# Kernel tuning notes

Measured on AMD Instinct MI355X. Metric: run time of the kernel, lower is better.

Reference implementation:

```python
import jax, jax.numpy as jnp
import numpy as np

B, S, HID = 4, 2048, 2048
H, KV, D = 16, 4, 128
ROT = 32  # partial rotary dim
EPS = 1e-6
NEG = -1e9


def _rms_norm(x, w):
    # Qwen3-Next RMSNorm: fp32 norm, (1 + weight) scaling
    xf = x.astype(jnp.float32)
    out = xf * jax.lax.rsqrt(jnp.mean(xf * xf, axis=-1, keepdims=True) + EPS)
    return (out * (1.0 + w.astype(jnp.float32))).astype(x.dtype)


def _rotate_half(x):
    x1, x2 = x[..., : x.shape[-1] // 2], x[..., x.shape[-1] // 2 :]
    return jnp.concatenate((-x2, x1), axis=-1)


def setup_inputs() -> dict:
    key = jax.random.key(0)
    ks = jax.random.split(key, 8)
    hidden_states = jax.random.normal(ks[0], (B, S, HID), dtype=jnp.float32)
    # real RoPE angles for the partial rotary dims
    inv_freq = 1.0 / (10000.0 ** (np.arange(0, ROT, 2, dtype=np.float32) / ROT))
    pos = np.arange(S, dtype=np.float32)
    freqs = np.einsum('s,d->sd', pos, inv_freq)          # [S, ROT/2]
    emb = np.concatenate([freqs, freqs], axis=-1)         # [S, ROT]
    cos = jnp.broadcast_to(jnp.asarray(np.cos(emb)), (B, S, ROT))
    sin = jnp.broadcast_to(jnp.asarray(np.sin(emb)), (B, S, ROT))
    # additive causal mask [B,1,S,S]
    causal = jnp.triu(jnp.full((S, S), NEG, dtype=jnp.float32), k=1)
    attention_mask = jnp.broadcast_to(causal[None, None], (B, 1, S, S))
    std = 0.02
    wq = jax.random.normal(ks[1], (HID, H * D * 2), dtype=jnp.float32) * std
    wk = jax.random.normal(ks[2], (HID, KV * D), dtype=jnp.float32) * std
    wv = jax.random.normal(ks[3], (HID, KV * D), dtype=jnp.float32) * std
    wo = jax.random.normal(ks[4], (H * D, HID), dtype=jnp.float32) * std
    q_norm_w = jax.random.normal(ks[5], (D,), dtype=jnp.float32) * std
    k_norm_w = jax.random.normal(ks[6], (D,), dtype=jnp.float32) * std
    return {
        'hidden_states': hidden_states, 'cos': cos, 'sin': sin,
        'attention_mask': attention_mask, 'wq': wq, 'wk': wk, 'wv': wv,
        'wo': wo, 'q_norm_w': q_norm_w, 'k_norm_w': k_norm_w,
    }


def reference(hidden_states, cos, sin, attention_mask, wq, wk, wv, wo, q_norm_w, k_norm_w):
    b, s, _ = hidden_states.shape
    scaling = D ** -0.5
    # q projection -> [B,S,H,2D]; split into query and gate (chunk dim=-1)
    qg = (hidden_states @ wq).reshape(b, s, H, 2 * D)
    q, gate = qg[..., :D], qg[..., D:]
    gate = gate.reshape(b, s, H * D)
    q = _rms_norm(q, q_norm_w).transpose(0, 2, 1, 3)                    # [B,H,S,D]
    k = _rms_norm((hidden_states @ wk).reshape(b, s, KV, D), k_norm_w).transpose(0, 2, 1, 3)
    v = (hidden_states @ wv).reshape(b, s, KV, D).transpose(0, 2, 1, 3)  # [B,KV,S,D]
    # partial RoPE on first ROT dims
    c, sn = cos[:, None], sin[:, None]                                   # [B,1,S,ROT]
    q_rot, q_pass = q[..., :ROT], q[..., ROT:]
    k_rot, k_pass = k[..., :ROT], k[..., ROT:]
    q = jnp.concatenate([q_rot * c + _rotate_half(q_rot) * sn, q_pass], axis=-1)
    k = jnp.concatenate([k_rot * c + _rotate_half(k_rot) * sn, k_pass], axis=-1)
    # GQA: repeat kv heads
    groups = H // KV
    k = jnp.repeat(k, groups, axis=1)
    v = jnp.repeat(v, groups, axis=1)
    scores = jnp.einsum('bhqd,bhkd->bhqk', q, k) * scaling + attention_mask
    probs = jax.nn.softmax(scores.astype(jnp.float32), axis=-1).astype(q.dtype)
    attn = jnp.einsum('bhqk,bhkd->bhqd', probs, v)
    attn = attn.transpose(0, 2, 1, 3).reshape(b, s, H * D)
    attn = attn * jax.nn.sigmoid(gate)
    return attn @ wo
```

## Files before the change

kernel.cpp:

```cpp
#include <hip/hip_runtime.h>

#define SEQ   2048
#define NHEAD 16
#define NKV   4
#define HDIM  128
#define NB    4
#define QKVW  5120

typedef unsigned short u16;
typedef unsigned int   u32;
typedef __bf16 v8bf __attribute__((ext_vector_type(8)));
typedef float  v4f  __attribute__((ext_vector_type(4)));

__device__ __forceinline__ u16 f2bf(float f) {
  u32 u = __float_as_uint(f);
  u += 0x7fffu + ((u >> 16) & 1u);
  return (u16)(u >> 16);
}
__device__ __forceinline__ float bf2f(u16 b) {
  return __uint_as_float(((u32)b) << 16);
}

__device__ __forceinline__ void gld_lds16(const u16* g, u16* l) {
  __builtin_amdgcn_global_load_lds(
      (const __attribute__((address_space(1))) u32*)(unsigned long long)(uintptr_t)g,
      (__attribute__((address_space(3))) u32*)(u32)(uintptr_t)l,
      16, 0, 0);
}

__global__ __launch_bounds__(256) void conv_f32_bf16(const float* __restrict__ s,
                                                     u16* __restrict__ d) {
  size_t i = ((size_t)blockIdx.x * 256 + threadIdx.x) * 8;
  float4 a = *(const float4*)(s + i);
  float4 b = *(const float4*)(s + i + 4);
  uint4 o;
  o.x = (u32)f2bf(a.x) | ((u32)f2bf(a.y) << 16);
  o.y = (u32)f2bf(a.z) | ((u32)f2bf(a.w) << 16);
  o.z = (u32)f2bf(b.x) | ((u32)f2bf(b.y) << 16);
  o.w = (u32)f2bf(b.z) | ((u32)f2bf(b.w) << 16);
  *(uint4*)(d + i) = o;
}

__global__ __launch_bounds__(256) void transpose_w(const float* __restrict__ src,
                                                   u16* __restrict__ dst,
                                                   int R, int C) {
  __shared__ u16 tile[64][80];
  int t = threadIdx.x;
  int r0 = blockIdx.y * 64, c0 = blockIdx.x * 64;
  int rr = t >> 2, cc = (t & 3) * 16;
  const float* sp = src + (size_t)(r0 + rr) * C + c0 + cc;
  float4 f0 = *(const float4*)sp;
  float4 f1 = *(const float4*)(sp + 4);
  float4 f2 = *(const float4*)(sp + 8);
  float4 f3 = *(const float4*)(sp + 12);
  u16* tp = &tile[rr][cc];
  tp[0] = f2bf(f0.x);  tp[1] = f2bf(f0.y);  tp[2] = f2bf(f0.z);  tp[3] = f2bf(f0.w);
  tp[4] = f2bf(f1.x);  tp[5] = f2bf(f1.y);  tp[6] = f2bf(f1.z);  tp[7] = f2bf(f1.w);
  tp[8] = f2bf(f2.x);  tp[9] = f2bf(f2.y);  tp[10] = f2bf(f2.z); tp[11] = f2bf(f2.w);
  tp[12] = f2bf(f3.x); tp[13] = f2bf(f3.y); tp[14] = f2bf(f3.z); tp[15] = f2bf(f3.w);
  __syncthreads();
  int cr = t >> 2, rc = (t & 3) * 16;
  u32 pk[8];
#pragma unroll
  for (int i = 0; i < 8; i++) {
    u32 lo = tile[rc + 2 * i][cr];
    u32 hi = tile[rc + 2 * i + 1][cr];
    pk[i] = lo | (hi << 16);
  }
  u16* dp = dst + (size_t)(c0 + cr) * R + r0 + rc;
  uint4 o0 = {pk[0], pk[1], pk[2], pk[3]};
  uint4 o1 = {pk[4], pk[5], pk[6], pk[7]};
  *(uint4*)dp       = o0;
  *(uint4*)(dp + 8) = o1;
}

__global__ __launch_bounds__(256) void transpose_v(const u16* __restrict__ qkv,
                                                   u16* __restrict__ vt) {
  __shared__ u16 tile[64][80];
  int t = threadIdx.x;
  int s0 = blockIdx.x * 64;
  int d0 = blockIdx.y * 64;
  int bg = blockIdx.z;
  int b = bg >> 2, g = bg & 3;
  int sr = t >> 2, dc = (t & 3) * 16;
  const u16* sp = qkv + (size_t)(b * SEQ + s0 + sr) * QKVW + 4608 + g * HDIM + d0 + dc;
  *(uint4*)&tile[sr][dc]     = *(const uint4*)sp;
  *(uint4*)&tile[sr][dc + 8] = *(const uint4*)(sp + 8);
  __syncthreads();
  int dr = t >> 2, sc = (t & 3) * 16;
  u32 pk[8];
#pragma unroll
  for (int i = 0; i < 8; i++) {
    u32 lo = tile[sc + 2 * i][dr];
    u32 hi = tile[sc + 2 * i + 1][dr];
    pk[i] = lo | (hi << 16);
  }
  u16* dp = vt + ((size_t)bg * HDIM + d0 + dr) * SEQ + s0 + sc;
  uint4 o0 = {pk[0], pk[1], pk[2], pk[3]};
  uint4 o1 = {pk[4], pk[5], pk[6], pk[7]};
  *(uint4*)dp       = o0;
  *(uint4*)(dp + 8) = o1;
}

template <bool OUT_F32>
__global__ __launch_bounds__(256) void gemm_bt(const u16* __restrict__ A,
                                               const u16* __restrict__ Bt,
                                               void* __restrict__ Cp,
                                               int M, int N, int K) {
  __shared__ u16 As[2][128 * 32];
  __shared__ u16 Bs[2][128 * 32];
  int tid  = threadIdx.x;
  int lane = tid & 63, wave = tid >> 6;
  int wr = wave >> 1, wc = wave & 1;
  int col = lane & 15, quad = lane >> 4;
  int m0 = blockIdx.y * 128, n0 = blockIdx.x * 128;

  v4f acc[4][4];
#pragma unroll
  for (int mi = 0; mi < 4; mi++)
#pragma unroll
    for (int ni = 0; ni < 4; ni++) acc[mi][ni] = (v4f){0.f, 0.f, 0.f, 0.f};

  int srow = tid >> 2;
  int skc  = (tid & 3) * 8;
  const u16* ag0 = A  + (size_t)(m0 + srow) * K + skc;
  const u16* ag1 = ag0 + (size_t)64 * K;
  const u16* bg0 = Bt + (size_t)(n0 + srow) * K + skc;
  const u16* bg1 = bg0 + (size_t)64 * K;

  gld_lds16(ag0, &As[0][tid * 8]);
  gld_lds16(ag1, &As[0][2048 + tid * 8]);
  gld_lds16(bg0, &Bs[0][tid * 8]);
  gld_lds16(bg1, &Bs[0][2048 + tid * 8]);
  __syncthreads();

  int nt = K >> 5;
  for (int t = 0; t < nt; ++t) {
    int cur = t & 1, nxt = cur ^ 1;
    if (t + 1 < nt) {
      int k0 = (t + 1) << 5;
      gld_lds16(ag0 + k0, &As[nxt][tid * 8]);
      gld_lds16(ag1 + k0, &As[nxt][2048 + tid * 8]);
      gld_lds16(bg0 + k0, &Bs[nxt][tid * 8]);
      gld_lds16(bg1 + k0, &Bs[nxt][2048 + tid * 8]);
    }
    v8bf a[4], bb[4];
#pragma unroll
    for (int mi = 0; mi < 4; mi++)
      a[mi] = *(const v8bf*)&As[cur][(wr * 64 + mi * 16 + col) * 32 + quad * 8];
#pragma unroll
    for (int ni = 0; ni < 4; ni++)
      bb[ni] = *(const v8bf*)&Bs[cur][(wc * 64 + ni * 16 + col) * 32 + quad * 8];
    __builtin_amdgcn_s_setprio(1);
#pragma unroll
    for (int mi = 0; mi < 4; mi++)
#pragma unroll
      for (int ni = 0; ni < 4; ni++)
        acc[mi][ni] = __builtin_amdgcn_mfma_f32_16x16x32_bf16(a[mi], bb[ni], acc[mi][ni], 0, 0, 0);
    __builtin_amdgcn_s_setprio(0);
    __syncthreads();
  }

#pragma unroll
  for (int mi = 0; mi < 4; mi++)
#pragma unroll
    for (int ni = 0; ni < 4; ni++) {
      int r_ = m0 + wr * 64 + mi * 16 + quad * 4;
      int c_ = n0 + wc * 64 + ni * 16 + col;
#pragma unroll
      for (int r = 0; r < 4; r++) {
        if (OUT_F32) ((float*)Cp)[(size_t)(r_ + r) * N + c_] = acc[mi][ni][r];
        else         ((u16*)Cp)[(size_t)(r_ + r) * N + c_]   = f2bf(acc[mi][ni][r]);
      }
    }
}

__global__ __launch_bounds__(256) void norm_rope(u16* __restrict__ qkv,
                                                 const float* __restrict__ cosb,
                                                 const float* __restrict__ sinb,
                                                 const float* __restrict__ qw,
                                                 const float* __restrict__ kw,
                                                 u16* __restrict__ kf) {
  int wave = threadIdx.x >> 6, lane = threadIdx.x & 63;
  int tw = blockIdx.x * 4 + wave;
  int token = tw / 20, r = tw % 20;
  const u16* src;
  u16* dst;
  const float* wptr;
  if (r < 16) {
    src  = qkv + (size_t)token * QKVW + r * 256;
    dst  = (u16*)src;
    wptr = qw;
  } else {
    src  = qkv + (size_t)token * QKVW + 4096 + (r - 16) * HDIM;
    int b = token >> 11, s = token & (SEQ - 1);
    dst  = kf + ((size_t)(b * NKV + (r - 16)) * SEQ + s) * HDIM;
    wptr = kw;
  }
  int d0 = lane * 2;
  u32 x = *(const u32*)(src + d0);
  float x0 = bf2f((u16)(x & 0xffff)), x1 = bf2f((u16)(x >> 16));
  float ss = x0 * x0 + x1 * x1;
#pragma unroll
  for (int off = 1; off < 64; off <<= 1) ss += __shfl_xor(ss, off, 64);
  float sc = rsqrtf(ss * (1.f / 128.f) + 1e-6f);
  float y0 = bf2f(f2bf(x0 * sc * (1.f + wptr[d0])));
  float y1 = bf2f(f2bf(x1 * sc * (1.f + wptr[d0 + 1])));
  float p0 = __shfl_xor(y0, 8, 64);
  float p1 = __shfl_xor(y1, 8, 64);
  float z0 = y0, z1 = y1;
  if (lane < 16) {
    float c0 = cosb[(size_t)token * 32 + d0];
    float c1 = cosb[(size_t)token * 32 + d0 + 1];
    float s0 = sinb[(size_t)token * 32 + d0];
    float s1 = sinb[(size_t)token * 32 + d0 + 1];
    if (lane < 8) { z0 = y0 * c0 - p0 * s0; z1 = y1 * c1 - p1 * s1; }
    else          { z0 = y0 * c0 + p0 * s0; z1 = y1 * c1 + p1 * s1; }
  }
  u32 outp = (u32)f2bf(z0) | ((u32)f2bf(z1) << 16);
  *(u32*)(dst + d0) = outp;
}

__global__ __launch_bounds__(512) void attn_kernel(const u16* __restrict__ qkv,
                                                   const u16* __restrict__ kf,
                                                   const u16* __restrict__ vt,
                                                   u16* __restrict__ ga) {
  __shared__ u16 ks[64 * 136];
  __shared__ u16 vs[128 * 88];
  int tid = threadIdx.x, lane = tid & 63, wave = tid >> 6;
  int col = lane & 15, quad = lane >> 4;
  int qt = 15 - blockIdx.x;
  int h = blockIdx.y, b = blockIdx.z;
  int g = h >> 2;
  int qw0 = qt * 128 + wave * 16;
  int myq = qw0 + col;
  const float scl2 = 0.08838834764831845f * 1.4426950408889634f;

  v8bf qfr[4];
  const u16* qbase = qkv + (size_t)(b * SEQ + myq) * QKVW + h * 256 + quad * 8;
#pragma unroll
  for (int kc = 0; kc < 4; kc++) qfr[kc] = *(const v8bf*)(qbase + kc * 32);

  v4f o[8];
#pragma unroll
  for (int nt = 0; nt < 8; nt++) o[nt] = (v4f){0.f, 0.f, 0.f, 0.f};
  float l = 0.f;
  float m = -1e30f;

  const u16* kfb = kf + (size_t)(b * NKV + g) * SEQ * HDIM;
  const u16* vtb = vt + (size_t)(b * NKV + g) * HDIM * SEQ;

  int ksr = tid >> 4, ksd = (tid & 15) * 8;
  int vsd = tid >> 3, w8 = tid & 7;
  int voff = 32 * ((w8 >> 2) & 1) + 16 * (w8 & 1) + 4 * ((w8 >> 1) & 1);
  int vsrc = w8 * 8;

  int nk = 2 * qt + 2;
  for (int it = 0; it < nk; it++) {
    int k0 = it * 64;
    __syncthreads();
#pragma unroll
    for (int p = 0; p < 2; p++)
      *(uint4*)&ks[(p * 32 + ksr) * 136 + ksd] =
          *(const uint4*)&kfb[(size_t)(k0 + p * 32 + ksr) * HDIM + ksd];
#pragma unroll
    for (int p = 0; p < 2; p++) {
      int d = p * 64 + vsd;
      uint4 gv = *(const uint4*)&vtb[(size_t)d * SEQ + k0 + vsrc];
      uint2 w0 = {gv.x, gv.y};
      uint2 w1 = {gv.z, gv.w};
      *(uint2*)&vs[d * 88 + voff]     = w0;
      *(uint2*)&vs[d * 88 + voff + 8] = w1;
    }
    __syncthreads();

    v4f st[4];
    __builtin_amdgcn_s_setprio(1);
#pragma unroll
    for (int t = 0; t < 4; t++) {
      v4f acc = (v4f){0.f, 0.f, 0.f, 0.f};
#pragma unroll
      for (int kc = 0; kc < 4; kc++) {
        v8bf kfr = *(const v8bf*)&ks[(t * 16 + col) * 136 + kc * 32 + quad * 8];
        acc = __builtin_amdgcn_mfma_f32_16x16x32_bf16(kfr, qfr[kc], acc, 0, 0, 0);
      }
      st[t] = acc;
    }
    __builtin_amdgcn_s_setprio(0);

    bool maskw = (k0 + 63 > qw0);
    float pmax = -1e30f;
#pragma unroll
    for (int t = 0; t < 4; t++)
#pragma unroll
      for (int r = 0; r < 4; r++) {
        float x = st[t][r] * scl2;
        if (maskw && (k0 + t * 16 + quad * 4 + r > myq)) x = -1e30f;
        st[t][r] = x;
        pmax = fmaxf(pmax, x);
      }
    pmax = fmaxf(pmax, __shfl_xor(pmax, 16, 64));
    pmax = fmaxf(pmax, __shfl_xor(pmax, 32, 64));
    if (__any(pmax > m + 8.f)) {
      float nm = fmaxf(m, pmax);
      float al = exp2f(m - nm);
      m = nm;
#pragma unroll
      for (int nt = 0; nt < 8; nt++)
#pragma unroll
        for (int r = 0; r < 4; r++) o[nt][r] *= al;
      l *= al;
    }
    v8bf pb0, pb1;
    float ls = 0.f;
#pragma unroll
    for (int t = 0; t < 4; t++)
#pragma unroll
      for (int r = 0; r < 4; r++) {
        float p = exp2f(st[t][r] - m);
        ls += p;
        if (t < 2) pb0[t * 4 + r] = (__bf16)p;
        else       pb1[(t - 2) * 4 + r] = (__bf16)p;
      }
    l += ls;

    __builtin_amdgcn_s_setprio(1);
#pragma unroll
    for (int nt = 0; nt < 8; nt++) {
      v8bf vb0 = *(const v8bf*)&vs[(nt * 16 + col) * 88 + quad * 8];
      v8bf vb1 = *(const v8bf*)&vs[(nt * 16 + col) * 88 + 32 + quad * 8];
      o[nt] = __builtin_amdgcn_mfma_f32_16x16x32_bf16(vb0, pb0, o[nt], 0, 0, 0);
      o[nt] = __builtin_amdgcn_mfma_f32_16x16x32_bf16(vb1, pb1, o[nt], 0, 0, 0);
    }
    __builtin_amdgcn_s_setprio(0);
  }

  l += __shfl_xor(l, 16, 64);
  l += __shfl_xor(l, 32, 64);
  float inv = 1.f / l;
  const u16* gb = qkv + (size_t)(b * SEQ + myq) * QKVW + h * 256 + 128 + quad * 4;
  u16* ob = ga + (size_t)(b * SEQ + myq) * 2048 + h * HDIM + quad * 4;
#pragma unroll
  for (int nt = 0; nt < 8; nt++) {
    uint2 gw = *(const uint2*)(gb + nt * 16);
    float g0 = bf2f((u16)(gw.x & 0xffff)), g1 = bf2f((u16)(gw.x >> 16));
    float g2 = bf2f((u16)(gw.y & 0xffff)), g3 = bf2f((u16)(gw.y >> 16));
    float a0 = o[nt][0] * inv * (1.f / (1.f + expf(-g0)));
    float a1 = o[nt][1] * inv * (1.f / (1.f + expf(-g1)));
    float a2 = o[nt][2] * inv * (1.f / (1.f + expf(-g2)));
    float a3 = o[nt][3] * inv * (1.f / (1.f + expf(-g3)));
    uint2 ow;
    ow.x = (u32)f2bf(a0) | ((u32)f2bf(a1) << 16);
    ow.y = (u32)f2bf(a2) | ((u32)f2bf(a3) << 16);
    *(uint2*)(ob + nt * 16) = ow;
  }
}

extern "C" void kernel_launch(void* const* d_in, const int* in_sizes, int n_in,
                              void* d_out, int out_size, void* d_ws, size_t ws_size,
                              hipStream_t stream) {
  const float* hidden = (const float*)d_in[0];
  const float* cosb   = (const float*)d_in[1];
  const float* sinb   = (const float*)d_in[2];
  const float* wq  = (const float*)d_in[4];
  const float* wk  = (const float*)d_in[5];
  const float* wv  = (const float*)d_in[6];
  const float* wo  = (const float*)d_in[7];
  const float* qnw = (const float*)d_in[8];
  const float* knw = (const float*)d_in[9];
  float* out = (float*)d_out;

  u16* ws      = (u16*)d_ws;
  u16* qkv_raw = ws;
  u16* region2 = qkv_raw + (size_t)8192 * QKVW;
  u16* region3 = region2 + (size_t)8192 * 2048;
  u16* hidden_bf = region2;
  u16* g_attn    = region2;
  u16* bt_qkv    = region3;
  u16* vt        = region3;
  u16* bt_wo     = region3 + (size_t)4194304;
  u16* k_f       = region3 + (size_t)8388608;

  conv_f32_bf16<<<dim3(8192), 256, 0, stream>>>(hidden, hidden_bf);
  transpose_w<<<dim3(64, 32), 256, 0, stream>>>(wq, bt_qkv, 2048, 4096);
  transpose_w<<<dim3(8, 32), 256, 0, stream>>>(wk, bt_qkv + (size_t)4096 * 2048, 2048, 512);
  transpose_w<<<dim3(8, 32), 256, 0, stream>>>(wv, bt_qkv + (size_t)4608 * 2048, 2048, 512);
  gemm_bt<false><<<dim3(QKVW / 128, 8192 / 128), 256, 0, stream>>>(hidden_bf, bt_qkv, qkv_raw, 8192, QKVW, 2048);
  norm_rope<<<dim3(8192 * 20 / 4), 256, 0, stream>>>(qkv_raw, cosb, sinb, qnw, knw, k_f);
  transpose_v<<<dim3(SEQ / 64, HDIM / 64, NB * NKV), 256, 0, stream>>>(qkv_raw, vt);
  transpose_w<<<dim3(32, 32), 256, 0, stream>>>(wo, bt_wo, 2048, 2048);
  attn_kernel<<<dim3(16, NHEAD, NB), 512, 0, stream>>>(qkv_raw, k_f, vt, g_attn);
  gemm_bt<true><<<dim3(2048 / 128, 8192 / 128), 256, 0, stream>>>(g_attn, bt_wo, out, 8192, 2048, 2048);
}
```

Before: 727.7 us.

## Enlarge GEMM tiles to 256x256 with triple-buffered LDS and XCD-aware block swizzle

Both projection GEMMs move from 128x128 tiles on 256 threads to 256x256 tiles on 512 threads, with each wave computing a 128x64 sub-tile. This raises arithmetic intensity per LDS load. A three-stage global-to-LDS pipeline with explicit vmcnt waits replaces double buffering and lets loads run two steps ahead. A 1-D grid is remapped so consecutive tiles go to the same XCD, for better L2 locality. The costs are more registers (32 accumulators per thread), 96KB of LDS per block, and fewer blocks: 640 for the QKV GEMM and only 256 for the output GEMM, which may underfill the 256 CUs.

Result: faster. 684.6 us (-5.9%).

```diff
diff --git a/kernel.cpp b/kernel.cpp
--- a/kernel.cpp
+++ b/kernel.cpp
@@ -103,69 +103,80 @@
 }
 
 template <bool OUT_F32>
-__global__ __launch_bounds__(256) void gemm_bt(const u16* __restrict__ A,
-                                               const u16* __restrict__ Bt,
-                                               void* __restrict__ Cp,
-                                               int M, int N, int K) {
-  __shared__ u16 As[2][128 * 32];
-  __shared__ u16 Bs[2][128 * 32];
+__global__ __launch_bounds__(512, 2) void gemm_bt(const u16* __restrict__ A,
+                                                  const u16* __restrict__ Bt,
+                                                  void* __restrict__ Cp,
+                                                  int M, int N, int K) {
+  __shared__ u16 As[3][256 * 32];
+  __shared__ u16 Bs[3][256 * 32];
   int tid  = threadIdx.x;
   int lane = tid & 63, wave = tid >> 6;
-  int wr = wave >> 1, wc = wave & 1;
+  int wr = wave >> 2, wc = wave & 3;
   int col = lane & 15, quad = lane >> 4;
-  int m0 = blockIdx.y * 128, n0 = blockIdx.x * 128;
-
-  v4f acc[4][4];
-#pragma unroll
-  for (int mi = 0; mi < 4; mi++)
+  int nwg = gridDim.x;
+  int cpx = nwg >> 3;
+  int id  = blockIdx.x;
+  int idp = (id & 7) * cpx + (id >> 3);
+  int ntile = N >> 8;
+  int m0 = (idp / ntile) << 8;
+  int n0 = (idp % ntile) << 8;
+
+  v4f acc[8][4];
+#pragma unroll
+  for (int mi = 0; mi < 8; mi++)
 #pragma unroll
     for (int ni = 0; ni < 4; ni++) acc[mi][ni] = (v4f){0.f, 0.f, 0.f, 0.f};
 
   int srow = tid >> 2;
   int skc  = (tid & 3) * 8;
-  const u16* ag0 = A  + (size_t)(m0 + srow) * K + skc;
-  const u16* ag1 = ag0 + (size_t)64 * K;
-  const u16* bg0 = Bt + (size_t)(n0 + srow) * K + skc;
-  const u16* bg1 = bg0 + (size_t)64 * K;
-
-  gld_lds16(ag0, &As[0][tid * 8]);
-  gld_lds16(ag1, &As[0][2048 + tid * 8]);
-  gld_lds16(bg0, &Bs[0][tid * 8]);
-  gld_lds16(bg1, &Bs[0][2048 + tid * 8]);
-  __syncthreads();
-
-  int nt = K >> 5;
-  for (int t = 0; t < nt; ++t) {
-    int cur = t & 1, nxt = cur ^ 1;
-    if (t + 1 < nt) {
-      int k0 = (t + 1) << 5;
-      gld_lds16(ag0 + k0, &As[nxt][tid * 8]);
-      gld_lds16(ag1 + k0, &As[nxt][2048 + tid * 8]);
-      gld_lds16(bg0 + k0, &Bs[nxt][tid * 8]);
-      gld_lds16(bg1 + k0, &Bs[nxt][2048 + tid * 8]);
-    }
-    v8bf a[4], bb[4];
-#pragma unroll
-    for (int mi = 0; mi < 4; mi++)
-      a[mi] = *(const v8bf*)&As[cur][(wr * 64 + mi * 16 + col) * 32 + quad * 8];
+  const u16* ag = A  + (size_t)(m0 + srow) * K + skc;
+  const u16* bg = Bt + (size_t)(n0 + srow) * K + skc;
+  const size_t rowK128 = (size_t)128 * K;
+
+#define STAGE(buf, k0)                                        \
+  do {                                                        \
+    gld_lds16(ag + (k0),           &As[buf][tid * 8]);        \
+    gld_lds16(ag + rowK128 + (k0), &As[buf][4096 + tid * 8]); \
+    gld_lds16(bg + (k0),           &Bs[buf][tid * 8]);        \
+    gld_lds16(bg + rowK128 + (k0), &Bs[buf][4096 + tid * 8]); \
+  } while (0)
+
+  STAGE(0, 0);
+  STAGE(1, 32);
+  asm volatile("s_waitcnt vmcnt(4)\n\ts_barrier" ::: "memory");
+
+  const int NT = K >> 5;
+  int cb = 0;
+  for (int t = 0; t < NT; ++t) {
+    int sb = cb + 2 >= 3 ? cb - 1 : cb + 2;
+    if (t + 2 < NT) {
+      int k0 = (t + 2) << 5;
+      STAGE(sb, k0);
+    }
+    v8bf bfr[4];
 #pragma unroll
     for (int ni = 0; ni < 4; ni++)
-      bb[ni] = *(const v8bf*)&Bs[cur][(wc * 64 + ni * 16 + col) * 32 + quad * 8];
+      bfr[ni] = *(const v8bf*)&Bs[cb][(wc * 64 + ni * 16 + col) * 32 + quad * 8];
     __builtin_amdgcn_s_setprio(1);
 #pragma unroll
-    for (int mi = 0; mi < 4; mi++)
+    for (int mi = 0; mi < 8; mi++) {
+      v8bf a = *(const v8bf*)&As[cb][(wr * 128 + mi * 16 + col) * 32 + quad * 8];
 #pragma unroll
       for (int ni = 0; ni < 4; ni++)
-        acc[mi][ni] = __builtin_amdgcn_mfma_f32_16x16x32_bf16(a[mi], bb[ni], acc[mi][ni], 0, 0, 0);
+        acc[mi][ni] = __builtin_amdgcn_mfma_f32_16x16x32_bf16(a, bfr[ni], acc[mi][ni], 0, 0, 0);
+    }
     __builtin_amdgcn_s_setprio(0);
-    __syncthreads();
-  }
-
-#pragma unroll
-  for (int mi = 0; mi < 4; mi++)
+    if (t < NT - 2) asm volatile("s_waitcnt vmcnt(4)\n\ts_barrier" ::: "memory");
+    else            asm volatile("s_waitcnt vmcnt(0)\n\ts_barrier" ::: "memory");
+    cb = cb + 1 >= 3 ? 0 : cb + 1;
+  }
+#undef STAGE
+
+#pragma unroll
+  for (int mi = 0; mi < 8; mi++)
 #pragma unroll
     for (int ni = 0; ni < 4; ni++) {
-      int r_ = m0 + wr * 64 + mi * 16 + quad * 4;
+      int r_ = m0 + wr * 128 + mi * 16 + quad * 4;
       int c_ = n0 + wc * 64 + ni * 16 + col;
 #pragma unroll
       for (int r = 0; r < 4; r++) {
@@ -385,10 +396,10 @@
   transpose_w<<<dim3(64, 32), 256, 0, stream>>>(wq, bt_qkv, 2048, 4096);
   transpose_w<<<dim3(8, 32), 256, 0, stream>>>(wk, bt_qkv + (size_t)4096 * 2048, 2048, 512);
   transpose_w<<<dim3(8, 32), 256, 0, stream>>>(wv, bt_qkv + (size_t)4608 * 2048, 2048, 512);
-  gemm_bt<false><<<dim3(QKVW / 128, 8192 / 128), 256, 0, stream>>>(hidden_bf, bt_qkv, qkv_raw, 8192, QKVW, 2048);
+  gemm_bt<false><<<dim3(640), 512, 0, stream>>>(hidden_bf, bt_qkv, qkv_raw, 8192, QKVW, 2048);
   norm_rope<<<dim3(8192 * 20 / 4), 256, 0, stream>>>(qkv_raw, cosb, sinb, qnw, knw, k_f);
   transpose_v<<<dim3(SEQ / 64, HDIM / 64, NB * NKV), 256, 0, stream>>>(qkv_raw, vt);
   transpose_w<<<dim3(32, 32), 256, 0, stream>>>(wo, bt_wo, 2048, 2048);
   attn_kernel<<<dim3(16, NHEAD, NB), 512, 0, stream>>>(qkv_raw, k_f, vt, g_attn);
-  gemm_bt<true><<<dim3(2048 / 128, 8192 / 128), 256, 0, stream>>>(g_attn, bt_wo, out, 8192, 2048, 2048);
-}
+  gemm_bt<true><<<dim3(256), 512, 0, stream>>>(g_attn, bt_wo, out, 8192, 2048, 2048);
+}
```
